# Kernel tuning notes

Measured on AMD Instinct MI355X. Metric: run time of the kernel, lower is better.

Reference implementation:

```python
import jax, jax.numpy as jnp
import numpy as np

D_MODEL = 1024
N_HEADS = 16
HEAD_DIM = D_MODEL // N_HEADS
B, LQ, LK = 4, 2048, 2048


def _rope(x, cos, sin):
    # x: (B, H, L, d); cos/sin: (B, 1, L, d)
    d = x.shape[-1]
    x1, x2 = x[..., : d // 2], x[..., d // 2 :]
    rotated = jnp.concatenate([-x2, x1], axis=-1)
    return x * cos + rotated * sin


def setup_inputs() -> dict:
    key = jax.random.key(0)
    ks = jax.random.split(key, 16)
    s = 1.0 / np.sqrt(D_MODEL)
    inp = {
        "query": jax.random.normal(ks[0], (B, LQ, D_MODEL), jnp.float32),
        "key": jax.random.normal(ks[1], (B, LK, D_MODEL), jnp.float32),
        "value": jax.random.normal(ks[2], (B, LK, D_MODEL), jnp.float32),
        "cos_q": jax.random.normal(ks[3], (B, LQ, HEAD_DIM), jnp.float32),
        "sin_q": jax.random.normal(ks[4], (B, LQ, HEAD_DIM), jnp.float32),
        "cos_k": jax.random.normal(ks[5], (B, LK, HEAD_DIM), jnp.float32),
        "sin_k": jax.random.normal(ks[6], (B, LK, HEAD_DIM), jnp.float32),
        "key_padding_mask": jnp.zeros((B, LK), dtype=bool),
        "Wq": jax.random.normal(ks[7], (D_MODEL, D_MODEL), jnp.float32) * s,
        "bq": jnp.zeros((D_MODEL,), jnp.float32),
        "Wk": jax.random.normal(ks[8], (D_MODEL, D_MODEL), jnp.float32) * s,
        "bk": jnp.zeros((D_MODEL,), jnp.float32),
        "Wv": jax.random.normal(ks[9], (D_MODEL, D_MODEL), jnp.float32) * s,
        "bv": jnp.zeros((D_MODEL,), jnp.float32),
        "Wo": jax.random.normal(ks[10], (D_MODEL, D_MODEL), jnp.float32) * s,
        "bo": jnp.zeros((D_MODEL,), jnp.float32),
    }
    return inp


def reference(query, key, value, cos_q, sin_q, cos_k, sin_k, key_padding_mask,
              Wq, bq, Wk, bk, Wv, bv, Wo, bo):
    Bq, Lq, _ = query.shape
    Lk = key.shape[1]
    scale = HEAD_DIM ** -0.5

    def proj(x, W, b, L):
        # torch Linear: x @ W.T + b, then (B, L, H, d) -> (B, H, L, d)
        y = jnp.einsum('ble,de->bld', x, W) + b
        return y.reshape(Bq, L, N_HEADS, HEAD_DIM).transpose(0, 2, 1, 3)

    q = proj(query, Wq, bq, Lq)
    k = proj(key, Wk, bk, Lk)
    v = proj(value, Wv, bv, Lk)

    q = _rope(q, cos_q[:, None, :Lq, :HEAD_DIM], sin_q[:, None, :Lq, :HEAD_DIM])
    k = _rope(k, cos_k[:, None, :Lk, :HEAD_DIM], sin_k[:, None, :Lk, :HEAD_DIM])

    attn = jnp.einsum('bhqd,bhkd->bhqk', q, k) * scale
    attn = jnp.where(key_padding_mask[:, None, None, :], -jnp.inf, attn)
    attn = jax.nn.softmax(attn, axis=-1)

    out = jnp.einsum('bhqk,bhkd->bhqd', attn, v)
    out = out.transpose(0, 2, 1, 3).reshape(Bq, Lq, D_MODEL)
    return jnp.einsum('ble,de->bld', out, Wo) + bo
```

## Files before the change

### kernel.cpp

```cpp
#include <hip/hip_runtime.h>
#include <hip/hip_bf16.h>
#include <stdint.h>
#include <stddef.h>

#define B_DIM 4
#define NH    16
#define LSEQ  2048
#define HD    64
#define DM    1024
#define TOKENS (B_DIM * LSEQ)

typedef __bf16 bf16_t;
typedef __attribute__((ext_vector_type(8))) __bf16 bf16x8;
typedef __attribute__((ext_vector_type(4))) __bf16 bf16x4;
typedef __attribute__((ext_vector_type(4))) float  f32x4;

#define GLD16(gp, lp) \
  __builtin_amdgcn_global_load_lds((__attribute__((address_space(1))) void*)(gp), \
                                   (__attribute__((address_space(3))) void*)(lp), 16, 0, 0)

#define WAITV6 asm volatile("s_waitcnt vmcnt(6)" ::: "memory")
#define WAITV4 asm volatile("s_waitcnt vmcnt(4)" ::: "memory")
#define WAITV0 asm volatile("s_waitcnt vmcnt(0)" ::: "memory")
#define WAITL0 asm volatile("s_waitcnt lgkmcnt(0)" ::: "memory")
#define SBAR   __builtin_amdgcn_s_barrier()
#define SCHED0 __builtin_amdgcn_sched_barrier(0)

__device__ __forceinline__ f32x4 mfma_16x16x32(bf16x8 a, bf16x8 b, f32x4 c) {
  return __builtin_amdgcn_mfma_f32_16x16x32_bf16(a, b, c, 0, 0, 0);
}

__global__ __launch_bounds__(256) void prep_kernel(const float* __restrict__ q,
                                                   const float* __restrict__ k,
                                                   const float* __restrict__ v,
                                                   const float* __restrict__ Wq,
                                                   const float* __restrict__ Wk,
                                                   const float* __restrict__ Wv,
                                                   const float* __restrict__ Wo,
                                                   const float* __restrict__ cos_q,
                                                   const float* __restrict__ sin_q,
                                                   const float* __restrict__ cos_k,
                                                   const float* __restrict__ sin_k,
                                                   bf16_t* __restrict__ xdst,
                                                   bf16_t* __restrict__ wdst,
                                                   float2* __restrict__ cs) {
  const int bid = blockIdx.x;
  const int tid = threadIdx.x;
  if (bid < 24576) {
    const int s = bid >> 13, off = bid & 8191;
    const float* src = (s == 0) ? q : (s == 1) ? k : v;
    const int i = (off * 256 + tid) * 4;
    const float4 val = *(const float4*)(src + i);
    bf16x4 o;
    o[0] = (bf16_t)val.x; o[1] = (bf16_t)val.y; o[2] = (bf16_t)val.z; o[3] = (bf16_t)val.w;
    *(bf16x4*)(xdst + (size_t)s * (TOKENS * (size_t)DM) + i) = o;
  } else if (bid < 28672) {
    const int s = (bid - 24576) >> 10, off = (bid - 24576) & 1023;
    const float* src = (s == 0) ? Wq : (s == 1) ? Wk : (s == 2) ? Wv : Wo;
    const int i = (off * 256 + tid) * 4;
    const float4 val = *(const float4*)(src + i);
    bf16x4 o;
    o[0] = (bf16_t)val.x; o[1] = (bf16_t)val.y; o[2] = (bf16_t)val.z; o[3] = (bf16_t)val.w;
    *(bf16x4*)(wdst + (size_t)s * (DM * (size_t)DM) + i) = o;
  } else {
    const int s = (bid - 28672) >> 9, off = (bid - 28672) & 511;
    const float* cp = (s == 0) ? cos_q : cos_k;
    const float* sp = (s == 0) ? sin_q : sin_k;
    const int i = (off * 256 + tid) * 4;
    const float4 c4 = *(const float4*)(cp + i);
    const float4 s4 = *(const float4*)(sp + i);
    float2* d = cs + (size_t)s * (TOKENS * (size_t)HD) + i;
    d[0] = make_float2(c4.x, s4.x);
    d[1] = make_float2(c4.y, s4.y);
    d[2] = make_float2(c4.z, s4.z);
    d[3] = make_float2(c4.w, s4.w);
  }
}

#define GEMM_TILE(CUR, WAIT, PRE, KK2)                                        \
  {                                                                           \
    WAIT; SBAR; SCHED0;                                                       \
    const bf16_t* Ac = &As[CUR][0];                                           \
    const bf16_t* Bc = &Bs[CUR][0];                                           \
    bf16x8 af[8], bfr[4];                                                     \
    _Pragma("unroll") for (int i_ = 0; i_ < 8; ++i_)                          \
      af[i_] = *(const bf16x8*)(Ac + (wm + i_ * 16 + l16) * 32 + fcol);       \
    _Pragma("unroll") for (int j_ = 0; j_ < 4; ++j_)                          \
      bfr[j_] = *(const bf16x8*)(Bc + (wn + j_ * 16 + l16) * 32 + fcol);      \
    _Pragma("unroll") for (int i_ = 0; i_ < 8; ++i_)                          \
      _Pragma("unroll") for (int j_ = 0; j_ < 4; ++j_)                        \
        acc[i_][j_] = mfma_16x16x32(af[i_], bfr[j_], acc[i_][j_]);            \
    WAITL0; SBAR; SCHED0;                                                     \
    if (PRE) {                                                                \
      const int kk2_ = (KK2);                                                 \
      GLD16(Ag0 + kk2_,            &As[CUR][0] + lA0);                        \
      GLD16(Ag0 + 64 * DM + kk2_,  &As[CUR][0] + lA1);                        \
      GLD16(Ag0 + 128 * DM + kk2_, &As[CUR][0] + lA2);                        \
      GLD16(Ag0 + 192 * DM + kk2_, &As[CUR][0] + lA3);                        \
      GLD16(Bg0 + kk2_,            &Bs[CUR][0] + lB0);                        \
      GLD16(Bg0 + 64 * DM + kk2_,  &Bs[CUR][0] + lB1);                        \
    }                                                                         \
  }

#define GEMM_STAGE(BUF, KK)                                                   \
  GLD16(Ag0 + (KK),            &As[BUF][0] + lA0);                            \
  GLD16(Ag0 + 64 * DM + (KK),  &As[BUF][0] + lA1);                            \
  GLD16(Ag0 + 128 * DM + (KK), &As[BUF][0] + lA2);                            \
  GLD16(Ag0 + 192 * DM + (KK), &As[BUF][0] + lA3);                            \
  GLD16(Bg0 + (KK),            &Bs[BUF][0] + lB0);                            \
  GLD16(Bg0 + 64 * DM + (KK),  &Bs[BUF][0] + lB1);

#define GEMM_LOOP                                                             \
  GEMM_STAGE(0, 0)                                                            \
  GEMM_STAGE(1, 32)                                                           \
  for (int ii = 0; ii < 15; ++ii) {                                           \
    const int kk2a = ii * 64 + 64;                                            \
    GEMM_TILE(0, WAITV6, true, kk2a);                                         \
    GEMM_TILE(1, WAITV6, true, kk2a + 32);                                    \
  }                                                                           \
  GEMM_TILE(0, WAITV6, false, 0);                                             \
  GEMM_TILE(1, WAITV0, false, 0);

#define GEMM_SETUP(APTR, BPTR)                                                \
  const int wave = tid >> 6, lane = tid & 63;                                 \
  const int quad = lane >> 4, l16 = lane & 15;                                \
  const int wm = (wave >> 1) * 128, wn = (wave & 1) * 64;                     \
  const int rb = wave * 16;                                                   \
  const int srow = rb + (lane >> 2);                                          \
  const int scol = ((lane & 3) ^ ((lane >> 3) & 3)) * 8;                      \
  const bf16_t* Ag0 = (APTR) + (size_t)(m0 + srow) * DM + scol;               \
  const bf16_t* Bg0 = (BPTR) + (size_t)(n0 + srow) * DM + scol;               \
  const int lA0 = srowlds, lA1 = srowlds + 64 * 32;                           \
  const int lA2 = srowlds + 128 * 32, lA3 = srowlds + 192 * 32;               \
  const int lB0 = srowlds, lB1 = srowlds + 64 * 32;                           \
  const int fcol = ((quad ^ ((l16 >> 1) & 3)) << 3);

__global__ __launch_bounds__(256, 2) void qkv_proj_kernel(const bf16_t* __restrict__ X,
                                                          const bf16_t* __restrict__ Wb,
                                                          const float* __restrict__ bq,
                                                          const float* __restrict__ bk,
                                                          const float* __restrict__ bv,
                                                          const float2* __restrict__ csq,
                                                          const float2* __restrict__ csk,
                                                          bf16_t* __restrict__ qtb,
                                                          bf16_t* __restrict__ ktb,
                                                          bf16_t* __restrict__ vtb) {
  __shared__ bf16_t As[2][256 * 32];
  __shared__ bf16_t Bs[2][128 * 32];
  const int z = blockIdx.z;
  const bf16_t* A  = X  + (size_t)z * TOKENS * DM;
  const bf16_t* Bw = Wb + (size_t)z * DM * DM;
  const float* bias = (z == 0) ? bq : (z == 1) ? bk : bv;

  const int tid = threadIdx.x;
  const int m0 = blockIdx.x * 256, n0 = blockIdx.y * 128;
  const int srowlds = (tid >> 6) * 16 * 32;

  f32x4 acc[8][4];
#pragma unroll
  for (int i = 0; i < 8; ++i)
#pragma unroll
    for (int j = 0; j < 4; ++j) acc[i][j] = (f32x4){0.f, 0.f, 0.f, 0.f};

  GEMM_SETUP(A, Bw)

  GEMM_LOOP

  if (z < 2) {
    const float2* cst = (z == 0) ? csq : csk;
    bf16_t* out = (z == 0) ? qtb : ktb;
    const int h = (n0 + wn) >> 6;
#pragma unroll
    for (int i = 0; i < 8; ++i) {
#pragma unroll
      for (int j = 0; j < 2; ++j) {
        const int hd1 = j * 16 + l16;
        const int hd2 = hd1 + 32;
        const float bn1 = bias[n0 + wn + hd1];
        const float bn2 = bias[n0 + wn + hd2];
#pragma unroll
        for (int r = 0; r < 4; ++r) {
          const int m = m0 + wm + i * 16 + quad * 4 + r;
          const int b = m >> 11, l = m & (LSEQ - 1);
          const size_t cb = ((size_t)b * LSEQ + l) * HD;
          const float x1 = (float)(bf16_t)(acc[i][j][r] + bn1);
          const float x2 = (float)(bf16_t)(acc[i][j + 2][r] + bn2);
          const float2 cs1 = cst[cb + hd1];
          const float2 cs2 = cst[cb + hd2];
          bf16_t* dst = out + (((size_t)(b * NH + h)) * LSEQ + l) * HD;
          dst[hd1] = (bf16_t)(x1 * cs1.x - x2 * cs1.y);
          dst[hd2] = (bf16_t)(x2 * cs2.x + x1 * cs2.y);
        }
      }
    }
  } else {
#pragma unroll
    for (int i = 0; i < 8; ++i) {
      const int mb = m0 + wm + i * 16 + quad * 4;
      const int b = mb >> 11, l = mb & (LSEQ - 1);
#pragma unroll
      for (int j = 0; j < 4; ++j) {
        const int n = n0 + wn + j * 16 + l16;
        const int h = n >> 6, hd = n & (HD - 1);
        const float bn = bias[n];
        bf16x4 pk;
#pragma unroll
        for (int r = 0; r < 4; ++r) pk[r] = (bf16_t)(acc[i][j][r] + bn);
        *(bf16x4*)(vtb + (((size_t)(b * NH + h)) * HD + hd) * LSEQ + l) = pk;
      }
    }
  }
}

__global__ __launch_bounds__(256, 2) void out_gemm_kernel(const bf16_t* __restrict__ A,
                                                          const bf16_t* __restrict__ Bw,
                                                          const float* __restrict__ bias,
                                                          float* __restrict__ out) {
  __shared__ bf16_t As[2][256 * 32];
  __shared__ bf16_t Bs[2][128 * 32];
  const int tid = threadIdx.x;
  const int m0 = blockIdx.x * 256, n0 = blockIdx.y * 128;
  const int srowlds = (tid >> 6) * 16 * 32;

  f32x4 acc[8][4];
#pragma unroll
  for (int i = 0; i < 8; ++i)
#pragma unroll
    for (int j = 0; j < 4; ++j) acc[i][j] = (f32x4){0.f, 0.f, 0.f, 0.f};

  GEMM_SETUP(A, Bw)

  GEMM_LOOP

#pragma unroll
  for (int i = 0; i < 8; ++i)
#pragma unroll
    for (int j = 0; j < 4; ++j) {
      const int n  = n0 + wn + j * 16 + l16;
      const float bn = bias[n];
#pragma unroll
      for (int r = 0; r < 4; ++r) {
        const int m = m0 + wm + i * 16 + quad * 4 + r;
        out[(size_t)m * DM + n] = acc[i][j][r] + bn;
      }
    }
}

#define ATTN_TILE(K0)                                                         \
  {                                                                           \
    const bf16_t* Kc = &Kl[cur][0];                                           \
    const bf16_t* Vc = &Vl[cur][0];                                           \
    f32x4 S[2][4];                                                            \
    _Pragma("unroll") for (int j = 0; j < 4; ++j) {                           \
      const bf16x8 kb0 = *(const bf16x8*)(Kc + oA + j * 1024);                \
      const bf16x8 kb1 = *(const bf16x8*)(Kc + oB + j * 1024);                \
      _Pragma("unroll") for (int u = 0; u < 2; ++u) {                         \
        f32x4 a = (f32x4){0.f, 0.f, 0.f, 0.f};                                \
        a = mfma_16x16x32(kb0, qa[u][0], a);                                  \
        a = mfma_16x16x32(kb1, qa[u][1], a);                                  \
        _Pragma("unroll") for (int r = 0; r < 4; ++r)                         \
          S[u][j][r] = __builtin_amdgcn_exp2f(a[r] * scale_l2e);              \
      }                                                                       \
    }                                                                         \
    if (has_mask) {                                                           \
      const uint64_t mlo = *(const uint64_t*)(mrow + (K0) + quad * 8);        \
      const uint64_t mhi = *(const uint64_t*)(mrow + (K0) + 32 + quad * 8);   \
      if (!__all((mlo | mhi) == 0)) {                                         \
        _Pragma("unroll") for (int j = 0; j < 4; ++j) {                       \
          const uint64_t mm = (j & 2) ? mhi : mlo;                            \
          _Pragma("unroll") for (int r = 0; r < 4; ++r)                       \
            if ((mm >> (((j & 1) * 4 + r) * 8)) & 0xff) {                     \
              S[0][j][r] = 0.f;                                               \
              S[1][j][r] = 0.f;                                               \
            }                                                                 \
        }                                                                     \
      }                                                                       \
    }                                                                         \
    bf16x8 pa[2][2];                                                          \
    _Pragma("unroll") for (int u = 0; u < 2; ++u)                             \
      _Pragma("unroll") for (int f = 0; f < 2; ++f)                           \
        _Pragma("unroll") for (int e = 0; e < 8; ++e)                         \
          pa[u][f][e] = (bf16_t)S[u][2 * f + (e >> 2)][e & 3];                \
    _Pragma("unroll") for (int u = 0; u < 2; ++u) {                           \
      Ol[u] = mfma_16x16x32(pa[u][0], ones, Ol[u]);                           \
      Ol[u] = mfma_16x16x32(pa[u][1], ones, Ol[u]);                           \
    }                                                                         \
    _Pragma("unroll") for (int jd = 0; jd < 4; ++jd) {                        \
      const bf16x8 vb0 = *(const bf16x8*)(Vc + oA + jd * 1024);               \
      const bf16x8 vb1 = *(const bf16x8*)(Vc + oB + jd * 1024);               \
      _Pragma("unroll") for (int u = 0; u < 2; ++u) {                         \
        O[u][jd] = mfma_16x16x32(pa[u][0], vb0, O[u][jd]);                    \
        O[u][jd] = mfma_16x16x32(pa[u][1], vb1, O[u][jd]);                    \
      }                                                                       \
    }                                                                         \
  }

__global__ __launch_bounds__(256, 4) void attn_kernel(const bf16_t* __restrict__ qt,
                                                      const bf16_t* __restrict__ kt,
                                                      const bf16_t* __restrict__ vt,
                                                      const unsigned char* __restrict__ mask,
                                                      bf16_t* __restrict__ ctx) {
  __shared__ bf16_t Kl[2][64 * 64];
  __shared__ bf16_t Vl[2][64 * 64];
  __shared__ int mflag;
  const int L  = blockIdx.x + (blockIdx.y << 4);
  const int bh = ((L & 7) << 3) | ((L >> 3) & 7);
  const int q0 = (L >> 6) * 128;
  const int b = bh >> 4, h = bh & (NH - 1);
  const int tid = threadIdx.x;
  const int wave = tid >> 6, lane = tid & 63;
  const int quad = lane >> 4, l16 = lane & 15;
  const float scale_l2e = 0.125f * 1.44269504f;

  const bf16_t* kbase = kt + (size_t)bh * LSEQ * HD;
  const bf16_t* vbase = vt + (size_t)bh * HD * LSEQ;
  const unsigned char* mrow = mask + (size_t)b * LSEQ;

  if (tid == 0) mflag = 0;
  __syncthreads();
  {
    const uint64_t mw = ((const uint64_t*)mrow)[tid];
    if (mw != 0) atomicOr(&mflag, 1);
  }

  bf16x8 qa[2][2];
#pragma unroll
  for (int u = 0; u < 2; ++u) {
    const bf16_t* qrow = qt + (((size_t)bh * LSEQ) + q0 + wave * 32 + u * 16 + l16) * HD;
    qa[u][0] = *(const bf16x8*)(qrow + quad * 8);
    qa[u][1] = *(const bf16x8*)(qrow + 32 + quad * 8);
  }

  f32x4 O[2][4];
  f32x4 Ol[2];
#pragma unroll
  for (int u = 0; u < 2; ++u) {
    Ol[u] = (f32x4){0.f, 0.f, 0.f, 0.f};
#pragma unroll
    for (int j = 0; j < 4; ++j) O[u][j] = (f32x4){0.f, 0.f, 0.f, 0.f};
  }
  bf16x8 ones;
#pragma unroll
  for (int e = 0; e < 8; ++e) ones[e] = (bf16_t)1.0f;

  const int srow8 = lane >> 3;
  const int scb   = lane & 7;
  const int c0 = wave * 2, c1 = c0 + 1;
  const int p0 = c0 * 8 + srow8, p1 = p0 + 8;
  const int g0 = (scb ^ srow8) * 8;
  const int sig0 = ((p0 >> 5) << 5) | (((p0 >> 2) & 3) << 3) | (((p0 >> 4) & 1) << 2) | (p0 & 3);
  const int sig1 = ((p1 >> 5) << 5) | (((p1 >> 2) & 3) << 3) | (((p1 >> 4) & 1) << 2) | (p1 & 3);
  const int kgo0 = sig0 * HD + g0, kgo1 = sig1 * HD + g0;
  const int vgo0 = p0 * LSEQ + g0, vgo1 = p1 * LSEQ + g0;
  const int ld0 = c0 * 512, ld1 = c1 * 512;

  const int sw  = l16 & 7;
  const int oA  = l16 * 64 + ((quad ^ sw) << 3);
  const int oB  = l16 * 64 + (((quad + 4) ^ sw) << 3);

  GLD16(kbase + kgo0, &Kl[0][0] + ld0);
  GLD16(kbase + kgo1, &Kl[0][0] + ld1);
  GLD16(vbase + vgo0, &Vl[0][0] + ld0);
  GLD16(vbase + vgo1, &Vl[0][0] + ld1);
  GLD16(kbase + (size_t)64 * HD + kgo0, &Kl[1][0] + ld0);
  GLD16(kbase + (size_t)64 * HD + kgo1, &Kl[1][0] + ld1);
  GLD16(vbase + (size_t)(vgo0 + 64), &Vl[1][0] + ld0);
  GLD16(vbase + (size_t)(vgo1 + 64), &Vl[1][0] + ld1);

  WAITL0; SBAR;
  const bool has_mask = (mflag != 0);

  int cur = 0;
  for (int t = 0; t < 30; ++t) {
    WAITV4; SBAR; SCHED0;
    ATTN_TILE(t * 64);
    WAITL0; SBAR; SCHED0;
    {
      const int k0n = t * 64 + 128;
      bf16_t* Kd = &Kl[cur][0];
      bf16_t* Vd = &Vl[cur][0];
      GLD16(kbase + (size_t)k0n * HD + kgo0, Kd + ld0);
      GLD16(kbase + (size_t)k0n * HD + kgo1, Kd + ld1);
      GLD16(vbase + (size_t)(vgo0 + k0n), Vd + ld0);
      GLD16(vbase + (size_t)(vgo1 + k0n), Vd + ld1);
    }
    cur ^= 1;
  }
  WAITV4; SBAR; SCHED0;
  ATTN_TILE(30 * 64);
  cur ^= 1;
  WAITV0; SBAR; SCHED0;
  ATTN_TILE(31 * 64);

#pragma unroll
  for (int u = 0; u < 2; ++u) {
    f32x4 linv;
#pragma unroll
    for (int r = 0; r < 4; ++r) linv[r] = 1.0f / Ol[u][r];
#pragma unroll
    for (int jd = 0; jd < 4; ++jd)
#pragma unroll
      for (int r = 0; r < 4; ++r) {
        const int l = q0 + wave * 32 + u * 16 + quad * 4 + r;
        const int d = h * HD + jd * 16 + l16;
        const float o = O[u][jd][r] * linv[r];
        ctx[((size_t)b * LSEQ + l) * DM + d] = (bf16_t)o;
      }
  }
}

extern "C" void kernel_launch(void* const* d_in, const int* in_sizes, int n_in,
                              void* d_out, int out_size, void* d_ws, size_t ws_size,
                              hipStream_t stream) {
  (void)in_sizes; (void)n_in; (void)out_size; (void)ws_size;
  const float* query = (const float*)d_in[0];
  const float* key   = (const float*)d_in[1];
  const float* value = (const float*)d_in[2];
  const float* cos_q = (const float*)d_in[3];
  const float* sin_q = (const float*)d_in[4];
  const float* cos_k = (const float*)d_in[5];
  const float* sin_k = (const float*)d_in[6];
  const unsigned char* mask = (const unsigned char*)d_in[7];
  const float* Wq = (const float*)d_in[8];
  const float* bq = (const float*)d_in[9];
  const float* Wk = (const float*)d_in[10];
  const float* bk = (const float*)d_in[11];
  const float* Wv = (const float*)d_in[12];
  const float* bv = (const float*)d_in[13];
  const float* Wo = (const float*)d_in[14];
  const float* bo = (const float*)d_in[15];
  float* out = (float*)d_out;

  const size_t ACT = (size_t)TOKENS * DM;
  const size_t WEL = (size_t)DM * DM;
  const size_t CSN = (size_t)TOKENS * HD;

  bf16_t* p   = (bf16_t*)d_ws;
  bf16_t* xq  = p; p += ACT;
  bf16_t* xk  = p; p += ACT;
  bf16_t* xv  = p; p += ACT;
  bf16_t* wqb = p; p += WEL;
  bf16_t* wkb = p; p += WEL;
  bf16_t* wvb = p; p += WEL;
  bf16_t* wob = p; p += WEL;
  bf16_t* qtb = p; p += ACT;
  bf16_t* ktb = p; p += ACT;
  bf16_t* vtb = p; p += ACT;
  bf16_t* ctx = xk;
  (void)xv; (void)wkb; (void)wvb;

  float2* csq = (float2*)out;
  float2* csk = csq + CSN;

  prep_kernel<<<dim3(29696), 256, 0, stream>>>(query, key, value, Wq, Wk, Wv, Wo,
                                               cos_q, sin_q, cos_k, sin_k,
                                               xq, wqb, csq);

  qkv_proj_kernel<<<dim3(TOKENS / 256, DM / 128, 3), 256, 0, stream>>>(
      xq, wqb, bq, bk, bv, csq, csk, qtb, ktb, vtb);

  attn_kernel<<<dim3(LSEQ / 128, B_DIM * NH), 256, 0, stream>>>(qtb, ktb, vtb, mask, ctx);

  out_gemm_kernel<<<dim3(TOKENS / 256, DM / 128), 256, 0, stream>>>(ctx, wob, bo, out);
}
```

Measured before the change: 360.3 us.

## Restructure projection GEMMs to 8 waves with BK=64 and interleaved staging

```diff
diff --git a/kernel.cpp b/kernel.cpp
--- a/kernel.cpp
+++ b/kernel.cpp
@@ -77,65 +77,75 @@
   }
 }
 
-#define GEMM_TILE(CUR, WAIT, PRE, KK2)                                        \
+#define STAGE_ROUND(DBUF, KK2, R)                                             \
+  if ((R) < 4) {                                                              \
+    GLD16(Ag0 + (size_t)(R) * 64 * DM + (KK2),                                \
+          Asb[DBUF] + ((R) * 64 + wave * 8) * 64);                            \
+  } else {                                                                    \
+    GLD16(Bg0 + (size_t)((R) - 4) * 64 * DM + (KK2),                          \
+          Bsb[DBUF] + (((R) - 4) * 64 + wave * 8) * 64);                      \
+  }
+
+#define KPH(CUR, KS, I, STG, KK2, R)                                          \
   {                                                                           \
-    WAIT; SBAR; SCHED0;                                                       \
-    const bf16_t* Ac = &As[CUR][0];                                           \
-    const bf16_t* Bc = &Bs[CUR][0];                                           \
-    bf16x8 af[8], bfr[4];                                                     \
-    _Pragma("unroll") for (int i_ = 0; i_ < 8; ++i_)                          \
-      af[i_] = *(const bf16x8*)(Ac + (wm + i_ * 16 + l16) * 32 + fcol);       \
-    _Pragma("unroll") for (int j_ = 0; j_ < 4; ++j_)                          \
-      bfr[j_] = *(const bf16x8*)(Bc + (wn + j_ * 16 + l16) * 32 + fcol);      \
-    _Pragma("unroll") for (int i_ = 0; i_ < 8; ++i_)                          \
-      _Pragma("unroll") for (int j_ = 0; j_ < 4; ++j_)                        \
-        acc[i_][j_] = mfma_16x16x32(af[i_], bfr[j_], acc[i_][j_]);            \
-    WAITL0; SBAR; SCHED0;                                                     \
-    if (PRE) {                                                                \
-      const int kk2_ = (KK2);                                                 \
-      GLD16(Ag0 + kk2_,            &As[CUR][0] + lA0);                        \
-      GLD16(Ag0 + 64 * DM + kk2_,  &As[CUR][0] + lA1);                        \
-      GLD16(Ag0 + 128 * DM + kk2_, &As[CUR][0] + lA2);                        \
-      GLD16(Ag0 + 192 * DM + kk2_, &As[CUR][0] + lA3);                        \
-      GLD16(Bg0 + kk2_,            &Bs[CUR][0] + lB0);                        \
-      GLD16(Bg0 + 64 * DM + kk2_,  &Bs[CUR][0] + lB1);                        \
+    const bf16x8 af_ = *(const bf16x8*)(Asb[CUR] + (wm + (I) * 16 + l16) * 64 \
+                                        + ((((KS) << 2) + quad) ^ sw8) * 8);  \
+    if ((I) == 0) {                                                           \
+      bfr[0] = *(const bf16x8*)(Bsb[CUR] + (wn + 0 + l16) * 64 + ((((KS) << 2) + quad) ^ sw8) * 8);  \
+      bfr[1] = *(const bf16x8*)(Bsb[CUR] + (wn + 16 + l16) * 64 + ((((KS) << 2) + quad) ^ sw8) * 8); \
+      bfr[2] = *(const bf16x8*)(Bsb[CUR] + (wn + 32 + l16) * 64 + ((((KS) << 2) + quad) ^ sw8) * 8); \
+      bfr[3] = *(const bf16x8*)(Bsb[CUR] + (wn + 48 + l16) * 64 + ((((KS) << 2) + quad) ^ sw8) * 8); \
     }                                                                         \
-  }
-
-#define GEMM_STAGE(BUF, KK)                                                   \
-  GLD16(Ag0 + (KK),            &As[BUF][0] + lA0);                            \
-  GLD16(Ag0 + 64 * DM + (KK),  &As[BUF][0] + lA1);                            \
-  GLD16(Ag0 + 128 * DM + (KK), &As[BUF][0] + lA2);                            \
-  GLD16(Ag0 + 192 * DM + (KK), &As[BUF][0] + lA3);                            \
-  GLD16(Bg0 + (KK),            &Bs[BUF][0] + lB0);                            \
-  GLD16(Bg0 + 64 * DM + (KK),  &Bs[BUF][0] + lB1);
-
-#define GEMM_LOOP                                                             \
-  GEMM_STAGE(0, 0)                                                            \
-  GEMM_STAGE(1, 32)                                                           \
-  for (int ii = 0; ii < 15; ++ii) {                                           \
-    const int kk2a = ii * 64 + 64;                                            \
-    GEMM_TILE(0, WAITV6, true, kk2a);                                         \
-    GEMM_TILE(1, WAITV6, true, kk2a + 32);                                    \
-  }                                                                           \
-  GEMM_TILE(0, WAITV6, false, 0);                                             \
-  GEMM_TILE(1, WAITV0, false, 0);
-
-#define GEMM_SETUP(APTR, BPTR)                                                \
+    if (STG) { STAGE_ROUND((CUR) ^ 1, KK2, R) }                               \
+    SBAR; WAITL0; SCHED0;                                                     \
+    __builtin_amdgcn_s_setprio(1);                                            \
+    acc[I][0] = mfma_16x16x32(af_, bfr[0], acc[I][0]);                        \
+    acc[I][1] = mfma_16x16x32(af_, bfr[1], acc[I][1]);                        \
+    acc[I][2] = mfma_16x16x32(af_, bfr[2], acc[I][2]);                        \
+    acc[I][3] = mfma_16x16x32(af_, bfr[3], acc[I][3]);                        \
+    __builtin_amdgcn_s_setprio(0);                                            \
+  }
+
+#define KTILE(CUR, KK, STG)                                                   \
+  {                                                                           \
+    bf16x8 bfr[4];                                                            \
+    KPH(CUR, 0, 0, STG, (KK) + 64, 0) SBAR;                                   \
+    KPH(CUR, 0, 1, STG, (KK) + 64, 1) SBAR;                                   \
+    KPH(CUR, 0, 2, STG, (KK) + 64, 2) SBAR;                                   \
+    KPH(CUR, 0, 3, STG, (KK) + 64, 3) SBAR;                                   \
+    KPH(CUR, 1, 0, STG, (KK) + 64, 4) SBAR;                                   \
+    KPH(CUR, 1, 1, STG, (KK) + 64, 5) SBAR;                                   \
+    KPH(CUR, 1, 2, false, 0, 0) SBAR;                                         \
+    KPH(CUR, 1, 3, false, 0, 0)                                               \
+  }
+
+#define GEMM8_SETUP(APTR, BPTR)                                               \
   const int wave = tid >> 6, lane = tid & 63;                                 \
   const int quad = lane >> 4, l16 = lane & 15;                                \
-  const int wm = (wave >> 1) * 128, wn = (wave & 1) * 64;                     \
-  const int rb = wave * 16;                                                   \
-  const int srow = rb + (lane >> 2);                                          \
-  const int scol = ((lane & 3) ^ ((lane >> 3) & 3)) * 8;                      \
-  const bf16_t* Ag0 = (APTR) + (size_t)(m0 + srow) * DM + scol;               \
-  const bf16_t* Bg0 = (BPTR) + (size_t)(n0 + srow) * DM + scol;               \
-  const int lA0 = srowlds, lA1 = srowlds + 64 * 32;                           \
-  const int lA2 = srowlds + 128 * 32, lA3 = srowlds + 192 * 32;               \
-  const int lB0 = srowlds, lB1 = srowlds + 64 * 32;                           \
-  const int fcol = ((quad ^ ((l16 >> 1) & 3)) << 3);
-
-__global__ __launch_bounds__(256, 2) void qkv_proj_kernel(const bf16_t* __restrict__ X,
+  const int wm = (wave >> 1) * 64, wn = (wave & 1) * 64;                      \
+  const int sw8 = l16 & 7;                                                    \
+  const int srow8 = lane >> 3;                                                \
+  const int sblk = ((lane & 7) ^ srow8) * 8;                                  \
+  const bf16_t* Ag0 = (APTR) + (size_t)(m0 + wave * 8 + srow8) * DM + sblk;   \
+  const bf16_t* Bg0 = (BPTR) + (size_t)(n0 + wave * 8 + srow8) * DM + sblk;   \
+  bf16_t* const Asb[2] = {&As[0][0], &As[1][0]};                              \
+  bf16_t* const Bsb[2] = {&Bs[0][0], &Bs[1][0]};
+
+#define GEMM8_LOOP                                                            \
+  STAGE_ROUND(0, 0, 0) STAGE_ROUND(0, 0, 1) STAGE_ROUND(0, 0, 2)              \
+  STAGE_ROUND(0, 0, 3) STAGE_ROUND(0, 0, 4) STAGE_ROUND(0, 0, 5)              \
+  STAGE_ROUND(1, 64, 0) STAGE_ROUND(1, 64, 1) STAGE_ROUND(1, 64, 2)           \
+  STAGE_ROUND(1, 64, 3) STAGE_ROUND(1, 64, 4) STAGE_ROUND(1, 64, 5)           \
+  WAITV6; SBAR;                                                               \
+  KTILE(0, 0, false) WAITV0; SBAR;                                            \
+  for (int tt = 0; tt < 7; ++tt) {                                            \
+    const int kk1 = tt * 128 + 64;                                            \
+    KTILE(1, kk1, true) WAITV0; SBAR;                                         \
+    KTILE(0, kk1 + 64, true) WAITV0; SBAR;                                    \
+  }                                                                           \
+  KTILE(1, 960, false)
+
+__global__ __launch_bounds__(512, 2) void qkv_proj_kernel(const bf16_t* __restrict__ X,
                                                           const bf16_t* __restrict__ Wb,
                                                           const float* __restrict__ bq,
                                                           const float* __restrict__ bk,
@@ -145,8 +155,8 @@
                                                           bf16_t* __restrict__ qtb,
                                                           bf16_t* __restrict__ ktb,
                                                           bf16_t* __restrict__ vtb) {
-  __shared__ bf16_t As[2][256 * 32];
-  __shared__ bf16_t Bs[2][128 * 32];
+  __shared__ bf16_t As[2][256 * 64];
+  __shared__ bf16_t Bs[2][128 * 64];
   const int z = blockIdx.z;
   const bf16_t* A  = X  + (size_t)z * TOKENS * DM;
   const bf16_t* Bw = Wb + (size_t)z * DM * DM;
@@ -154,24 +164,23 @@
 
   const int tid = threadIdx.x;
   const int m0 = blockIdx.x * 256, n0 = blockIdx.y * 128;
-  const int srowlds = (tid >> 6) * 16 * 32;
-
-  f32x4 acc[8][4];
-#pragma unroll
-  for (int i = 0; i < 8; ++i)
+
+  f32x4 acc[4][4];
+#pragma unroll
+  for (int i = 0; i < 4; ++i)
 #pragma unroll
     for (int j = 0; j < 4; ++j) acc[i][j] = (f32x4){0.f, 0.f, 0.f, 0.f};
 
-  GEMM_SETUP(A, Bw)
-
-  GEMM_LOOP
+  GEMM8_SETUP(A, Bw)
+
+  GEMM8_LOOP
 
   if (z < 2) {
     const float2* cst = (z == 0) ? csq : csk;
     bf16_t* out = (z == 0) ? qtb : ktb;
     const int h = (n0 + wn) >> 6;
 #pragma unroll
-    for (int i = 0; i < 8; ++i) {
+    for (int i = 0; i < 4; ++i) {
 #pragma unroll
       for (int j = 0; j < 2; ++j) {
         const int hd1 = j * 16 + l16;
@@ -195,7 +204,7 @@
     }
   } else {
 #pragma unroll
-    for (int i = 0; i < 8; ++i) {
+    for (int i = 0; i < 4; ++i) {
       const int mb = m0 + wm + i * 16 + quad * 4;
       const int b = mb >> 11, l = mb & (LSEQ - 1);
 #pragma unroll
@@ -212,28 +221,27 @@
   }
 }
 
-__global__ __launch_bounds__(256, 2) void out_gemm_kernel(const bf16_t* __restrict__ A,
+__global__ __launch_bounds__(512, 2) void out_gemm_kernel(const bf16_t* __restrict__ A,
                                                           const bf16_t* __restrict__ Bw,
                                                           const float* __restrict__ bias,
                                                           float* __restrict__ out) {
-  __shared__ bf16_t As[2][256 * 32];
-  __shared__ bf16_t Bs[2][128 * 32];
+  __shared__ bf16_t As[2][256 * 64];
+  __shared__ bf16_t Bs[2][128 * 64];
   const int tid = threadIdx.x;
   const int m0 = blockIdx.x * 256, n0 = blockIdx.y * 128;
-  const int srowlds = (tid >> 6) * 16 * 32;
-
-  f32x4 acc[8][4];
-#pragma unroll
-  for (int i = 0; i < 8; ++i)
+
+  f32x4 acc[4][4];
+#pragma unroll
+  for (int i = 0; i < 4; ++i)
 #pragma unroll
     for (int j = 0; j < 4; ++j) acc[i][j] = (f32x4){0.f, 0.f, 0.f, 0.f};
 
-  GEMM_SETUP(A, Bw)
-
-  GEMM_LOOP
-
-#pragma unroll
-  for (int i = 0; i < 8; ++i)
+  GEMM8_SETUP(A, Bw)
+
+  GEMM8_LOOP
+
+#pragma unroll
+  for (int i = 0; i < 4; ++i)
 #pragma unroll
     for (int j = 0; j < 4; ++j) {
       const int n  = n0 + wn + j * 16 + l16;
@@ -456,10 +464,10 @@
                                                cos_q, sin_q, cos_k, sin_k,
                                                xq, wqb, csq);
 
-  qkv_proj_kernel<<<dim3(TOKENS / 256, DM / 128, 3), 256, 0, stream>>>(
+  qkv_proj_kernel<<<dim3(TOKENS / 256, DM / 128, 3), 512, 0, stream>>>(
       xq, wqb, bq, bk, bv, csq, csk, qtb, ktb, vtb);
 
   attn_kernel<<<dim3(LSEQ / 128, B_DIM * NH), 256, 0, stream>>>(qtb, ktb, vtb, mask, ctx);
 
-  out_gemm_kernel<<<dim3(TOKENS / 256, DM / 128), 256, 0, stream>>>(ctx, wob, bo, out);
-}
+  out_gemm_kernel<<<dim3(TOKENS / 256, DM / 128), 512, 0, stream>>>(ctx, wob, bo, out);
+}
```

New measurement: 367.8 us. 1.02x slower.
